# Performance work log

Measured on AMD Instinct MI355X. Metric: run time of the kernel, lower is better.

The kernel has to match this reference:

```python
import jax, jax.numpy as jnp
from jax import lax
import numpy as np

B, N, K, H = 8, 4096, 24, 32  # graphs, nodes/graph, kNN k, hidden_dim


def setup_inputs() -> dict:
    key = jax.random.key(0)
    ks = jax.random.split(key, 16)
    W = lambda k, i, o: jax.random.normal(k, (i, o), jnp.float32) * 0.1
    b = lambda k, o: jax.random.normal(k, (o,), jnp.float32) * 0.01
    inp = {
        'x_lc': jax.random.normal(ks[0], (B * N, 4), jnp.float32),
        'batch_lc': jnp.repeat(jnp.arange(B, dtype=jnp.int64), N),
        'enc_w1': W(ks[1], 4, H), 'enc_b1': b(ks[2], H),
        'enc_w2': W(ks[3], H, H), 'enc_b2': b(ks[4], H),
        'conv1_w': W(ks[5], 2 * H, H), 'conv1_b': b(ks[6], H),
        'conv2_w': W(ks[7], 2 * H, H), 'conv2_b': b(ks[8], H),
        'conv3_w': W(ks[9], 2 * H, H), 'conv3_b': b(ks[10], H),
        'out_w1': W(ks[11], H, 32), 'out_b1': b(ks[12], 32),
        'out_w2': W(ks[13], 32, 16), 'out_b2': b(ks[14], 16),
        'out_w3': W(ks[15], 16, 8), 'out_b3': jnp.zeros((8,), jnp.float32),
    }
    return inp


def _dynamic_edge_conv(x, w, bias):
    # x: [B, N, D]; kNN within each graph, edge msg nn([x_i, x_j - x_i]), max-agg
    d2 = jnp.sum(x * x, axis=-1)  # [B, N]
    dist = d2[:, :, None] + d2[:, None, :] - 2.0 * jnp.einsum('bnd,bmd->bnm', x, x)
    # kNN index computation is non-differentiable (as in PyG knn)
    idx = lax.top_k(-lax.stop_gradient(dist), K)[1]  # [B, N, K], includes self
    xj = jax.vmap(lambda xb, ib: xb[ib])(x, idx)  # [B, N, K, D]
    xi = jnp.broadcast_to(x[:, :, None, :], xj.shape)
    e = jnp.concatenate([xi, xj - xi], axis=-1)  # [B, N, K, 2D]
    h = jax.nn.elu(e @ w + bias)  # [B, N, K, H]
    return jnp.max(h, axis=2)  # [B, N, H]


def reference(x_lc, batch_lc, enc_w1, enc_b1, enc_w2, enc_b2,
              conv1_w, conv1_b, conv2_w, conv2_b, conv3_w, conv3_b,
              out_w1, out_b1, out_w2, out_b2, out_w3, out_b3):
    # lc_encode
    h = jax.nn.elu(x_lc @ enc_w1 + enc_b1)
    h = jax.nn.elu(h @ enc_w2 + enc_b2)  # [B*N, H]
    h = h.reshape(B, N, H)  # equal-sized sorted graphs
    h = _dynamic_edge_conv(h, conv1_w, conv1_b)
    h = _dynamic_edge_conv(h, conv2_w, conv2_b)
    h = _dynamic_edge_conv(h, conv3_w, conv3_b)
    h = h.reshape(B * N, H)
    o = jax.nn.elu(h @ out_w1 + out_b1)
    o = jax.nn.elu(o @ out_w2 + out_b2)
    o = o @ out_w3 + out_b3  # [B*N, 8]
    return (o, batch_lc)
```

## Files before the change

kernel.cpp:

```cpp
#include <hip/hip_runtime.h>
#include <cstddef>
#include <cstdint>

#define BN    32768
#define NG    4096
#define KNN   24
#define KPW   14
#define KM    32
#define CHK   128
#define NBQ   64
#define STKD  16
#define TRIG  13

typedef float f32x4_t __attribute__((ext_vector_type(4)));
typedef short s16x8_t __attribute__((ext_vector_type(8)));

__device__ __forceinline__ float elu_f(float x) {
    return x > 0.f ? x : expm1f(x);
}

__device__ __forceinline__ unsigned short f2bf(float f) {
    unsigned u = __float_as_uint(f);
    unsigned r = (u + 0x7FFFu + ((u >> 16) & 1u)) >> 16;
    return (unsigned short)r;
}

__device__ __forceinline__ void gload_lds16(const void* g, void* l) {
    __builtin_amdgcn_global_load_lds(
        (const __attribute__((address_space(1))) unsigned*)g,
        (__attribute__((address_space(3))) unsigned*)l, 16, 0, 0);
}

__device__ __forceinline__ void pack_node(int n, const float* hv,
    unsigned short* __restrict__ hbf, unsigned short* __restrict__ til,
    float* __restrict__ d2b)
{
    __align__(16) unsigned short us[32];
    float s = 0.f;
#pragma unroll
    for (int k = 0; k < 32; ++k) {
        us[k] = f2bf(hv[k]);
        float v = __uint_as_float(((unsigned)us[k]) << 16);
        s = fmaf(v, v, s);
    }
    d2b[n] = s;
    const uint4* up = reinterpret_cast<const uint4*>(us);
    uint4* lp = reinterpret_cast<uint4*>(hbf + (size_t)n * 32);
#pragma unroll
    for (int j = 0; j < 4; ++j) lp[j] = up[j];
    const int g = n >> 12, ln = n & 4095, tile = ln >> 4, c = ln & 15;
    unsigned short* tb = til + (size_t)g * 131072 + tile * 512 + c * 8;
#pragma unroll
    for (int kg = 0; kg < 4; ++kg)
        *reinterpret_cast<uint4*>(tb + kg * 128) = up[kg];
}

__global__ __launch_bounds__(128) void k_encoder(
    const float* __restrict__ x,
    const float* __restrict__ w1, const float* __restrict__ b1,
    const float* __restrict__ w2, const float* __restrict__ b2,
    float* __restrict__ hOut, float* __restrict__ d2Out,
    unsigned short* __restrict__ hbf, unsigned short* __restrict__ til,
    float* __restrict__ d2b)
{
    __shared__ float sw1[4 * 32];
    __shared__ float sb1[32];
    __shared__ float sw2[32 * 32];
    __shared__ float sb2[32];
    int tid = threadIdx.x;
    sw1[tid] = w1[tid];
    if (tid < 32) sb1[tid] = b1[tid];
    for (int i = tid; i < 1024; i += 128) sw2[i] = w2[i];
    if (tid >= 32 && tid < 64) sb2[tid - 32] = b2[tid - 32];
    __syncthreads();

    int node = blockIdx.x * 128 + tid;
    float4 xv = reinterpret_cast<const float4*>(x)[node];

    float h1[32];
#pragma unroll
    for (int o = 0; o < 32; ++o) {
        float s = sb1[o];
        s = fmaf(xv.x, sw1[o], s);
        s = fmaf(xv.y, sw1[32 + o], s);
        s = fmaf(xv.z, sw1[64 + o], s);
        s = fmaf(xv.w, sw1[96 + o], s);
        h1[o] = elu_f(s);
    }
    float h2[32];
    float d2 = 0.f;
#pragma unroll
    for (int o = 0; o < 32; ++o) {
        float s = sb2[o];
#pragma unroll
        for (int f = 0; f < 32; ++f) s = fmaf(h1[f], sw2[f * 32 + o], s);
        float v = elu_f(s);
        h2[o] = v;
        d2 = fmaf(v, v, d2);
    }
    float4* hp = reinterpret_cast<float4*>(hOut) + (size_t)node * 8;
#pragma unroll
    for (int j = 0; j < 8; ++j)
        hp[j] = make_float4(h2[4 * j], h2[4 * j + 1], h2[4 * j + 2], h2[4 * j + 3]);
    d2Out[node] = d2;
    pack_node(node, h2, hbf, til, d2b);
}

#define CHAIN14(nk_) do { \
    unsigned nk = (nk_); \
    _Pragma("unroll") \
    for (int jj = 0; jj < KPW; ++jj) { \
        unsigned tj = top[jj]; \
        unsigned lo = nk < tj ? nk : tj; \
        unsigned hi = nk < tj ? tj : nk; \
        top[jj] = lo; nk = hi; \
    } \
} while (0)

__global__ __launch_bounds__(512, 4) void k_scan(
    const unsigned short* __restrict__ til,
    const unsigned short* __restrict__ hbf,
    const float* __restrict__ d2b,
    unsigned short* __restrict__ mgs)
{
    __shared__ __align__(16) unsigned char smem[49152];
    constexpr int SD2 = 0;
    constexpr int STK = 16384;
    constexpr int LST = 16384;

    const int tid = threadIdx.x;
    const int lane = tid & 63;
    const int wid = __builtin_amdgcn_readfirstlane(tid >> 6);
    const int qt = wid >> 1;
    const int par = wid & 1;
    const int bid = blockIdx.x;
    const int g = bid >> 6;
    const int gbase = g << 12;
    const int blockq = (bid & 63) * NBQ;
    const int qnode = gbase + blockq + qt * 16 + (lane & 15);
    const int rg = (lane >> 4) * 4;

    gload_lds16(d2b + gbase + wid * 256 + lane * 4, smem + SD2 + wid * 1024);
    gload_lds16(d2b + gbase + 2048 + wid * 256 + lane * 4,
                smem + SD2 + 8192 + wid * 1024);

    s16x8_t bfrag = *reinterpret_cast<const s16x8_t*>(
        hbf + (size_t)qnode * 32 + (lane >> 4) * 8);
    const float qd2 = d2b[qnode];
    const float nqd2h = -0.5f * qd2;

    unsigned top[KPW];
#pragma unroll
    for (int j = 0; j < KPW; ++j) top[j] = 0xFFFFFFFFu;
    unsigned thresh = 0xFFFFFFFFu;
    int pcnt = 0;

    const char* gtw = (const char*)til + (size_t)g * 262144
                    + (size_t)par * 1024 + (size_t)lane * 16;
    const float* d2s = reinterpret_cast<const float*>(smem + SD2);
    unsigned* stkl = reinterpret_cast<unsigned*>(smem + STK + wid * 4096) + lane;

    __syncthreads();

    s16x8_t af[4];
#pragma unroll
    for (int i = 0; i < 4; ++i)
        af[i] = *reinterpret_cast<const s16x8_t*>(gtw + i * 2048);

    for (int c = 0; c < 32; ++c) {
        s16x8_t an[4];
        if (c < 31) {
#pragma unroll
            for (int i = 0; i < 4; ++i)
                an[i] = *reinterpret_cast<const s16x8_t*>(
                    gtw + (size_t)(c + 1) * 8192 + i * 2048);
        } else {
#pragma unroll
            for (int i = 0; i < 4; ++i) an[i] = af[i];
        }
        f32x4_t cv[4];
#pragma unroll
        for (int i = 0; i < 4; ++i)
            cv[i] = *reinterpret_cast<const f32x4_t*>(
                d2s + c * 128 + (i * 2 + par) * 16 + rg);
#pragma unroll
        for (int i = 0; i < 4; ++i) {
            const int t = i * 2 + par;
            f32x4_t acc;
#pragma unroll
            for (int r = 0; r < 4; ++r) acc[r] = fmaf(-0.5f, cv[i][r], nqd2h);
            acc = __builtin_amdgcn_mfma_f32_16x16x32_bf16(af[i], bfrag, acc, 0, 0, 0);
            const int cid0 = c * CHK + t * 16 + rg;
#pragma unroll
            for (int r = 0; r < 4; ++r) {
                unsigned key = (__float_as_uint(acc[r]) & 0xFFFFF000u)
                             | (unsigned)(cid0 + r);
                stkl[pcnt * 64] = key;
                pcnt += (key < thresh) ? 1 : 0;
            }
            if (__any(pcnt >= TRIG)) {
#pragma unroll 1
                for (int j = 0; j < STKD; ++j) {
                    if (!__any(pcnt > j)) break;
                    unsigned kk = stkl[j * 64];
                    unsigned k = (j < pcnt) ? kk : 0xFFFFFFFFu;
                    CHAIN14(k);
                }
                pcnt = 0;
                thresh = top[KPW - 1];
            }
        }
#pragma unroll
        for (int i = 0; i < 4; ++i) af[i] = an[i];
    }
#pragma unroll 1
    for (int j = 0; j < STKD; ++j) {
        if (!__any(pcnt > j)) break;
        unsigned kk = stkl[j * 64];
        unsigned k = (j < pcnt) ? kk : 0xFFFFFFFFu;
        CHAIN14(k);
    }
    __syncthreads();

    unsigned* lst = reinterpret_cast<unsigned*>(smem + LST);
#pragma unroll
    for (int j = 0; j < KPW; ++j) lst[(wid * 64 + lane) * KPW + j] = top[j];
    __syncthreads();

    if (wid != 0) return;

    {
        const int q = tid;
        unsigned mt[KM];
#pragma unroll
        for (int j = 0; j < KM; ++j) mt[j] = 0xFFFFFFFFu;
        for (int li = 0; li < 8; ++li) {
            const unsigned* lk = lst +
                (((q >> 4) * 2 + (li >> 2)) * 64 + (li & 3) * 16 + (q & 15)) * KPW;
            for (int j = 0; j < KPW; ++j) {
                unsigned key = lk[j];
                if (key >= mt[KM - 1]) break;
                unsigned nk = key;
#pragma unroll
                for (int jj = 0; jj < KM; ++jj) {
                    unsigned tj = mt[jj];
                    unsigned lo = nk < tj ? nk : tj;
                    unsigned hi = nk < tj ? tj : nk;
                    mt[jj] = lo; nk = hi;
                }
            }
        }
        unsigned short* mrow = mgs + (size_t)(gbase + blockq + q) * 32;
#pragma unroll
        for (int s = 0; s < KM; ++s)
            mrow[s] = (unsigned short)(mt[s] & 0xFFFu);
    }
}

__global__ __launch_bounds__(128) void k_refine(
    const unsigned short* __restrict__ mgs,
    const float* __restrict__ hf,
    const float* __restrict__ d2x,
    const float* __restrict__ cw, const float* __restrict__ cb,
    int* __restrict__ idxOut,
    float* __restrict__ Abuf, float* __restrict__ Bbuf)
{
    __shared__ float sw[2048];
    __shared__ float sb[32];
    __shared__ __align__(16) float dstv[16][36];
    __shared__ int mgl[16][32];

    const int tid = threadIdx.x;
    const int bid = blockIdx.x;
    const int g = bid >> 8;
    const int gbase = g << 12;
    const int blockq = (bid & 255) * 16;

    for (int i = tid; i < 2048; i += 128) sw[i] = cw[i];
    if (tid < 32) sb[tid] = cb[tid];
    for (int i = tid; i < 512; i += 128)
        mgl[i >> 5][i & 31] =
            (int)mgs[(size_t)(gbase + blockq + (i >> 5)) * 32 + (i & 31)];
    __syncthreads();

    const int q  = tid >> 3;
    const int s0 = tid & 7;
    const int qn = gbase + blockq + q;

    const float4* qp = reinterpret_cast<const float4*>(hf) + (size_t)qn * 8;
    float4 qf[8];
#pragma unroll
    for (int j = 0; j < 8; ++j) qf[j] = qp[j];
    const float qd2e = d2x[qn];
    int cids[4];
#pragma unroll
    for (int ss = 0; ss < 4; ++ss) {
        const int s = s0 + ss * 8;
        const int cid = mgl[q][s];
        cids[ss] = cid;
        const int cn = gbase + cid;
        const float4* cp = reinterpret_cast<const float4*>(hf) + (size_t)cn * 8;
        float ax = 0.f, ay = 0.f, az = 0.f, aw = 0.f;
#pragma unroll
        for (int jj = 0; jj < 8; ++jj) {
            float4 cc = cp[jj];
            ax = fmaf(qf[jj].x, cc.x, ax);
            ay = fmaf(qf[jj].y, cc.y, ay);
            az = fmaf(qf[jj].z, cc.z, az);
            aw = fmaf(qf[jj].w, cc.w, aw);
        }
        float dot = (ax + ay) + (az + aw);
        dstv[q][s] = fmaf(-2.f, dot, qd2e + d2x[cn]);
    }
    __syncthreads();

    {
        float dsr[32];
        const float4* dvp = reinterpret_cast<const float4*>(dstv[q]);
#pragma unroll
        for (int jj = 0; jj < 8; ++jj) {
            float4 t = dvp[jj];
            dsr[4 * jj] = t.x; dsr[4 * jj + 1] = t.y;
            dsr[4 * jj + 2] = t.z; dsr[4 * jj + 3] = t.w;
        }
        int* o = idxOut + (size_t)qn * KNN;
#pragma unroll
        for (int ss = 0; ss < 4; ++ss) {
            const int s = s0 + ss * 8;
            const float di = dsr[s];
            int rank = 0;
#pragma unroll
            for (int j = 0; j < 32; ++j)
                rank += (dsr[j] < di || (dsr[j] == di && j < s)) ? 1 : 0;
            if (rank < KNN) o[rank] = cids[ss];
        }
    }

    {
        const int o0 = s0 * 4;
        float hreg[32];
#pragma unroll
        for (int j = 0; j < 8; ++j) {
            float4 v = qp[j];
            hreg[4 * j] = v.x; hreg[4 * j + 1] = v.y;
            hreg[4 * j + 2] = v.z; hreg[4 * j + 3] = v.w;
        }
        float4 s1 = make_float4(0.f, 0.f, 0.f, 0.f);
        float4 s2 = make_float4(0.f, 0.f, 0.f, 0.f);
#pragma unroll
        for (int f = 0; f < 32; ++f) {
            float hv = hreg[f];
            float4 wa = *reinterpret_cast<const float4*>(sw + f * 32 + o0);
            float4 wb = *reinterpret_cast<const float4*>(sw + (32 + f) * 32 + o0);
            s1.x = fmaf(hv, wa.x, s1.x); s1.y = fmaf(hv, wa.y, s1.y);
            s1.z = fmaf(hv, wa.z, s1.z); s1.w = fmaf(hv, wa.w, s1.w);
            s2.x = fmaf(hv, wb.x, s2.x); s2.y = fmaf(hv, wb.y, s2.y);
            s2.z = fmaf(hv, wb.z, s2.z); s2.w = fmaf(hv, wb.w, s2.w);
        }
        float4 bv = *reinterpret_cast<const float4*>(sb + o0);
        float4 av = make_float4(s1.x - s2.x + bv.x, s1.y - s2.y + bv.y,
                                s1.z - s2.z + bv.z, s1.w - s2.w + bv.w);
        *reinterpret_cast<float4*>(Abuf + (size_t)qn * 32 + o0) = av;
        *reinterpret_cast<float4*>(Bbuf + (size_t)qn * 32 + o0) = s2;
    }
}

template <bool LAST>
__global__ __launch_bounds__(128) void k_aggregate(
    const float* __restrict__ A, const float* __restrict__ Bv,
    const int* __restrict__ idx,
    float* __restrict__ hOut, float* __restrict__ d2Out,
    unsigned short* __restrict__ hbf, unsigned short* __restrict__ til,
    float* __restrict__ d2b,
    const float* __restrict__ w1, const float* __restrict__ b1,
    const float* __restrict__ w2, const float* __restrict__ b2,
    const float* __restrict__ w3, const float* __restrict__ b3,
    float* __restrict__ out)
{
    __shared__ float sw1[1024];
    __shared__ float sb1[32];
    __shared__ float sw2[512];
    __shared__ float sb2[16];
    __shared__ float sw3[128];
    __shared__ float sb3[8];
    int tid = threadIdx.x;
    if (LAST) {
        for (int i = tid; i < 1024; i += 128) sw1[i] = w1[i];
        for (int i = tid; i < 512; i += 128) sw2[i] = w2[i];
        sw3[tid] = w3[tid];
        if (tid < 32) sb1[tid] = b1[tid];
        if (tid >= 32 && tid < 48) sb2[tid - 32] = b2[tid - 32];
        if (tid >= 48 && tid < 56) sb3[tid - 48] = b3[tid - 48];
        __syncthreads();
    }

    int node = blockIdx.x * 128 + tid;
    int g = node >> 12;
    const int* ip = idx + (size_t)node * KNN;

    float4 m[8];
#pragma unroll
    for (int j = 0; j < 8; ++j) m[j] = make_float4(-1e30f, -1e30f, -1e30f, -1e30f);

    for (int k = 0; k < KNN; ++k) {
        int cand = (g << 12) + ip[k];
        const float4* bp = reinterpret_cast<const float4*>(Bv) + (size_t)cand * 8;
#pragma unroll
        for (int j = 0; j < 8; ++j) {
            float4 b = bp[j];
            m[j].x = fmaxf(m[j].x, b.x);
            m[j].y = fmaxf(m[j].y, b.y);
            m[j].z = fmaxf(m[j].z, b.z);
            m[j].w = fmaxf(m[j].w, b.w);
        }
    }
    const float4* ap = reinterpret_cast<const float4*>(A) + (size_t)node * 8;
    float hv[32];
    float d2 = 0.f;
#pragma unroll
    for (int j = 0; j < 8; ++j) {
        float4 a = ap[j];
        float4 v;
        v.x = elu_f(a.x + m[j].x);
        v.y = elu_f(a.y + m[j].y);
        v.z = elu_f(a.z + m[j].z);
        v.w = elu_f(a.w + m[j].w);
        d2 = fmaf(v.x, v.x, d2);
        d2 = fmaf(v.y, v.y, d2);
        d2 = fmaf(v.z, v.z, d2);
        d2 = fmaf(v.w, v.w, d2);
        hv[4 * j] = v.x; hv[4 * j + 1] = v.y; hv[4 * j + 2] = v.z; hv[4 * j + 3] = v.w;
    }

    if (!LAST) {
        float4* hp = reinterpret_cast<float4*>(hOut) + (size_t)node * 8;
#pragma unroll
        for (int j = 0; j < 8; ++j)
            hp[j] = make_float4(hv[4 * j], hv[4 * j + 1], hv[4 * j + 2], hv[4 * j + 3]);
        d2Out[node] = d2;
        pack_node(node, hv, hbf, til, d2b);
    } else {
        float o1[32];
#pragma unroll
        for (int o = 0; o < 32; ++o) {
            float s = sb1[o];
#pragma unroll
            for (int f = 0; f < 32; ++f) s = fmaf(hv[f], sw1[f * 32 + o], s);
            o1[o] = elu_f(s);
        }
        float o2[16];
#pragma unroll
        for (int o = 0; o < 16; ++o) {
            float s = sb2[o];
#pragma unroll
            for (int f = 0; f < 32; ++f) s = fmaf(o1[f], sw2[f * 16 + o], s);
            o2[o] = elu_f(s);
        }
        float o3[8];
#pragma unroll
        for (int o = 0; o < 8; ++o) {
            float s = sb3[o];
#pragma unroll
            for (int f = 0; f < 16; ++f) s = fmaf(o2[f], sw3[f * 8 + o], s);
            o3[o] = s;
        }
        float4* op = reinterpret_cast<float4*>(out) + (size_t)node * 2;
        op[0] = make_float4(o3[0], o3[1], o3[2], o3[3]);
        op[1] = make_float4(o3[4], o3[5], o3[6], o3[7]);
        out[(size_t)BN * 8 + node] = (float)(node >> 12);
    }
}

extern "C" void kernel_launch(void* const* d_in, const int* in_sizes, int n_in,
                              void* d_out, int out_size, void* d_ws, size_t ws_size,
                              hipStream_t stream)
{
    (void)in_sizes; (void)n_in; (void)out_size; (void)ws_size;
    const float* x      = (const float*)d_in[0];
    const float* enc_w1 = (const float*)d_in[2];
    const float* enc_b1 = (const float*)d_in[3];
    const float* enc_w2 = (const float*)d_in[4];
    const float* enc_b2 = (const float*)d_in[5];
    const float* conv_w[3] = { (const float*)d_in[6], (const float*)d_in[8], (const float*)d_in[10] };
    const float* conv_b[3] = { (const float*)d_in[7], (const float*)d_in[9], (const float*)d_in[11] };
    const float* out_w1 = (const float*)d_in[12];
    const float* out_b1 = (const float*)d_in[13];
    const float* out_w2 = (const float*)d_in[14];
    const float* out_b2 = (const float*)d_in[15];
    const float* out_w3 = (const float*)d_in[16];
    const float* out_b3 = (const float*)d_in[17];

    char* ws = (char*)d_ws;
    float*          hA   = (float*)(ws + 0);
    float*          hB   = (float*)(ws + 4194304);
    unsigned short* hbfA = (unsigned short*)(ws + 8388608);
    unsigned short* hbfB = (unsigned short*)(ws + 10485760);
    unsigned short* tilA = (unsigned short*)(ws + 12582912);
    unsigned short* tilB = (unsigned short*)(ws + 14680064);
    float*          d2A  = (float*)(ws + 16777216);
    float*          d2B  = (float*)(ws + 16908288);
    float*          d2bA = (float*)(ws + 17039360);
    float*          d2bB = (float*)(ws + 17170432);
    int*            idx  = (int*)(ws + 17301504);
    float*          Abuf = (float*)(ws + 20447232);
    float*          Bbuf = (float*)(ws + 24641536);

    k_encoder<<<256, 128, 0, stream>>>(x, enc_w1, enc_b1, enc_w2, enc_b2,
                                       hA, d2A, hbfA, tilA, d2bA);

    float* hin = hA;   float* d2in = d2A;   float* d2bin = d2bA;
    unsigned short* hbfin = hbfA; unsigned short* tilin = tilA;
    float* hout = hB;  float* d2out = d2B;  float* d2bout = d2bB;
    unsigned short* hbfout = hbfB; unsigned short* tilout = tilB;

    for (int l = 0; l < 3; ++l) {
        unsigned short* mgs = tilout;
        k_scan<<<512, 512, 0, stream>>>(tilin, hbfin, d2bin, mgs);
        k_refine<<<2048, 128, 0, stream>>>(mgs, hin, d2in,
                                           conv_w[l], conv_b[l], idx, Abuf, Bbuf);
        if (l < 2) {
            k_aggregate<false><<<256, 128, 0, stream>>>(
                Abuf, Bbuf, idx, hout, d2out, hbfout, tilout, d2bout,
                nullptr, nullptr, nullptr, nullptr, nullptr, nullptr, nullptr);
        } else {
            k_aggregate<true><<<256, 128, 0, stream>>>(
                Abuf, Bbuf, idx, nullptr, nullptr, nullptr, nullptr, nullptr,
                out_w1, out_b1, out_w2, out_b2, out_w3, out_b3, (float*)d_out);
        }
        float* tf; unsigned short* ts;
        tf = hin; hin = hout; hout = tf;
        tf = d2in; d2in = d2out; d2out = tf;
        tf = d2bin; d2bin = d2bout; d2bout = tf;
        ts = hbfin; hbfin = hbfout; hbfout = ts;
        ts = tilin; tilin = tilout; tilout = ts;
    }
}
```

Measured before the change: 587.2 us.

## Parallelize kNN candidate merge by rank counting across all warps; shuffle-based refine ranking

```diff
diff --git a/kernel.cpp b/kernel.cpp
--- a/kernel.cpp
+++ b/kernel.cpp
@@ -117,6 +117,9 @@
     } \
 } while (0)
 
+#define LBASE(q, li) \
+    (((((q) >> 4) * 2 + ((li) >> 2)) * 64 + ((li) & 3) * 16 + ((q) & 15)))
+
 __global__ __launch_bounds__(512, 4) void k_scan(
     const unsigned short* __restrict__ til,
     const unsigned short* __restrict__ hbf,
@@ -227,33 +230,31 @@
     for (int j = 0; j < KPW; ++j) lst[(wid * 64 + lane) * KPW + j] = top[j];
     __syncthreads();
 
-    if (wid != 0) return;
-
     {
-        const int q = tid;
-        unsigned mt[KM];
-#pragma unroll
-        for (int j = 0; j < KM; ++j) mt[j] = 0xFFFFFFFFu;
-        for (int li = 0; li < 8; ++li) {
-            const unsigned* lk = lst +
-                (((q >> 4) * 2 + (li >> 2)) * 64 + (li & 3) * 16 + (q & 15)) * KPW;
-            for (int j = 0; j < KPW; ++j) {
-                unsigned key = lk[j];
-                if (key >= mt[KM - 1]) break;
-                unsigned nk = key;
-#pragma unroll
-                for (int jj = 0; jj < KM; ++jj) {
-                    unsigned tj = mt[jj];
-                    unsigned lo = nk < tj ? nk : tj;
-                    unsigned hi = nk < tj ? tj : nk;
-                    mt[jj] = lo; nk = hi;
-                }
+        const int q  = tid >> 3;
+        const int li = tid & 7;
+        const unsigned* myl = lst + LBASE(q, li) * KPW;
+        unsigned mine[KPW];
+        int rk[KPW];
+#pragma unroll
+        for (int j = 0; j < KPW; ++j) { mine[j] = myl[j]; rk[j] = j; }
+        const unsigned myMax = mine[KPW - 1];
+#pragma unroll 1
+        for (int u = 1; u < 8; ++u) {
+            const int lj = (li + u) & 7;
+            const unsigned* pl = lst + LBASE(q, lj) * KPW;
+#pragma unroll 1
+            for (int k = 0; k < KPW; ++k) {
+                unsigned pk = pl[k];
+                if (pk >= myMax) break;
+#pragma unroll
+                for (int j = 0; j < KPW; ++j) rk[j] += (pk < mine[j]) ? 1 : 0;
             }
         }
         unsigned short* mrow = mgs + (size_t)(gbase + blockq + q) * 32;
 #pragma unroll
-        for (int s = 0; s < KM; ++s)
-            mrow[s] = (unsigned short)(mt[s] & 0xFFFu);
+        for (int j = 0; j < KPW; ++j)
+            if (rk[j] < KM) mrow[rk[j]] = (unsigned short)(mine[j] & 0xFFFu);
     }
 }
 
@@ -267,8 +268,6 @@
 {
     __shared__ float sw[2048];
     __shared__ float sb[32];
-    __shared__ __align__(16) float dstv[16][36];
-    __shared__ int mgl[16][32];
 
     const int tid = threadIdx.x;
     const int bid = blockIdx.x;
@@ -278,9 +277,6 @@
 
     for (int i = tid; i < 2048; i += 128) sw[i] = cw[i];
     if (tid < 32) sb[tid] = cb[tid];
-    for (int i = tid; i < 512; i += 128)
-        mgl[i >> 5][i & 31] =
-            (int)mgs[(size_t)(gbase + blockq + (i >> 5)) * 32 + (i & 31)];
     __syncthreads();
 
     const int q  = tid >> 3;
@@ -292,11 +288,13 @@
 #pragma unroll
     for (int j = 0; j < 8; ++j) qf[j] = qp[j];
     const float qd2e = d2x[qn];
+
     int cids[4];
+    float d[4];
 #pragma unroll
     for (int ss = 0; ss < 4; ++ss) {
         const int s = s0 + ss * 8;
-        const int cid = mgl[q][s];
+        const int cid = (int)mgs[(size_t)qn * 32 + s];
         cids[ss] = cid;
         const int cn = gbase + cid;
         const float4* cp = reinterpret_cast<const float4*>(hf) + (size_t)cn * 8;
@@ -310,30 +308,42 @@
             aw = fmaf(qf[jj].w, cc.w, aw);
         }
         float dot = (ax + ay) + (az + aw);
-        dstv[q][s] = fmaf(-2.f, dot, qd2e + d2x[cn]);
-    }
-    __syncthreads();
+        d[ss] = fmaf(-2.f, dot, qd2e + d2x[cn]);
+    }
 
     {
-        float dsr[32];
-        const float4* dvp = reinterpret_cast<const float4*>(dstv[q]);
-#pragma unroll
-        for (int jj = 0; jj < 8; ++jj) {
-            float4 t = dvp[jj];
-            dsr[4 * jj] = t.x; dsr[4 * jj + 1] = t.y;
-            dsr[4 * jj + 2] = t.z; dsr[4 * jj + 3] = t.w;
+        int rk[4];
+#pragma unroll
+        for (int i = 0; i < 4; ++i) {
+            int r = 0;
+#pragma unroll
+            for (int j = 0; j < 4; ++j) {
+                if (j != i)
+                    r += (d[j] < d[i] || (d[j] == d[i] && j < i)) ? 1 : 0;
+            }
+            rk[i] = r;
+        }
+#pragma unroll
+        for (int t = 1; t < 8; ++t) {
+            float pd[4];
+#pragma unroll
+            for (int ss = 0; ss < 4; ++ss) pd[ss] = __shfl_xor(d[ss], t);
+            const int ps0 = s0 ^ t;
+#pragma unroll
+            for (int i = 0; i < 4; ++i) {
+                const int mys = s0 + 8 * i;
+#pragma unroll
+                for (int ss = 0; ss < 4; ++ss) {
+                    const int pss = ps0 + 8 * ss;
+                    rk[i] += (pd[ss] < d[i] ||
+                              (pd[ss] == d[i] && pss < mys)) ? 1 : 0;
+                }
+            }
         }
         int* o = idxOut + (size_t)qn * KNN;
 #pragma unroll
-        for (int ss = 0; ss < 4; ++ss) {
-            const int s = s0 + ss * 8;
-            const float di = dsr[s];
-            int rank = 0;
-#pragma unroll
-            for (int j = 0; j < 32; ++j)
-                rank += (dsr[j] < di || (dsr[j] == di && j < s)) ? 1 : 0;
-            if (rank < KNN) o[rank] = cids[ss];
-        }
+        for (int i = 0; i < 4; ++i)
+            if (rk[i] < KNN) o[rk[i]] = cids[i];
     }
 
     {
@@ -341,9 +351,8 @@
         float hreg[32];
 #pragma unroll
         for (int j = 0; j < 8; ++j) {
-            float4 v = qp[j];
-            hreg[4 * j] = v.x; hreg[4 * j + 1] = v.y;
-            hreg[4 * j + 2] = v.z; hreg[4 * j + 3] = v.w;
+            hreg[4 * j]     = qf[j].x; hreg[4 * j + 1] = qf[j].y;
+            hreg[4 * j + 2] = qf[j].z; hreg[4 * j + 3] = qf[j].w;
         }
         float4 s1 = make_float4(0.f, 0.f, 0.f, 0.f);
         float4 s2 = make_float4(0.f, 0.f, 0.f, 0.f);
```

After: 554.1 us. 5.6% less time.
